# Kernel optimization log

Measured on AMD Instinct MI355X. Metric: run time of the kernel, lower is better.

The kernel has to match this reference:

```python
import jax, jax.numpy as jnp
import numpy as np

N = 100000          # neurons
MAX_DELAY = 5
NSYN = 5            # synaptic basis functions
T = 20              # timesteps
B = 1
E_REC = 2_000_000
N_LGN = 17400
E_LGN = 600_000
N_BKG = 100
E_BKG = 200_000
DT = 1.0
DAMPENING = 0.3
REC_DAMPENING = 0.4


@jax.custom_vjp
def spike(v_scaled, damp):
    return (v_scaled > 0.0).astype(v_scaled.dtype)

def _spike_fwd(v_scaled, damp):
    return spike(v_scaled, damp), (v_scaled, damp)

def _spike_bwd(res, dy):
    v_scaled, damp = res
    dv = dy * damp * jnp.maximum(1.0 - jnp.abs(v_scaled), 0.0)
    return dv, jnp.zeros_like(damp)

spike.defvjp(_spike_fwd, _spike_bwd)


def _sparse_current(spk, idx, w, fac, n_out):
    # spk: [B, S]; idx: [E, 2] (post, pre); w: [E]; fac: [E, NSYN] -> [B, n_out, NSYN]
    vals = spk[:, idx[:, 1]]                                 # [B, E] gather
    contrib = vals[:, :, None] * (w[:, None] * fac)[None]    # [B, E, NSYN]
    seg = lambda c: jax.ops.segment_sum(c, idx[:, 0], num_segments=n_out)
    return jax.vmap(seg)(contrib)


def setup_inputs():
    key = jax.random.key(0)
    ks = jax.random.split(key, 24)
    lgn_spikes = (jax.random.uniform(ks[0], (T, B, N_LGN)) < 0.05).astype(jnp.float32)
    bkg_spikes = (jax.random.uniform(ks[1], (T, B, N_BKG)) < 0.10).astype(jnp.float32)
    post = jax.random.randint(ks[2], (E_REC,), 0, N)
    pre = jax.random.randint(ks[3], (E_REC,), 0, N)
    delay = jax.random.randint(ks[4], (E_REC,), 1, MAX_DELAY + 1)
    rec_indices = jnp.stack([post, pre + N * (delay - 1)], axis=1)  # delayed column offset
    rec_w = jax.random.normal(ks[5], (E_REC,)) * 0.01
    rec_factors = jax.random.uniform(ks[6], (E_REC, NSYN))
    lgn_indices = jnp.stack([jax.random.randint(ks[7], (E_LGN,), 0, N),
                             jax.random.randint(ks[8], (E_LGN,), 0, N_LGN)], axis=1)
    lgn_w = jnp.abs(jax.random.normal(ks[9], (E_LGN,))) * 0.02
    lgn_factors = jax.random.uniform(ks[10], (E_LGN, NSYN))
    bkg_indices = jnp.stack([jax.random.randint(ks[11], (E_BKG,), 0, N),
                             jax.random.randint(ks[12], (E_BKG,), 0, N_BKG)], axis=1)
    bkg_w = jnp.abs(jax.random.normal(ks[13], (E_BKG,))) * 0.02
    bkg_factors = jax.random.uniform(ks[14], (E_BKG, NSYN))
    # GLIF neuron params in normalized voltage units (E_L=0, V_th=1 after scaling)
    tau = jax.random.uniform(ks[15], (N,)) * 30.0 + 10.0      # membrane tau (ms)
    c_m = jax.random.uniform(ks[16], (N,)) * 150.0 + 50.0     # capacitance
    decay = jnp.exp(-DT / tau)
    current_factor = (1.0 - decay) * tau / c_m
    v_reset = jnp.zeros((N,), jnp.float32)
    t_ref = jax.random.uniform(ks[17], (N,)) * 3.0 + 1.0
    k = jax.random.uniform(ks[18], (N, 2)) * 0.3 + 0.003      # ASC decay rates
    asc_amps = jax.random.normal(ks[19], (N, 2)) * 0.01
    v_th = jnp.ones((N,), jnp.float32)
    normalizer = jnp.ones((N,), jnp.float32)                   # v_th - e_l
    gathered_g = jnp.zeros((N,), jnp.float32)                  # g * e_l (= 0 normalized)
    tau_syn = jnp.array([5.5, 8.5, 2.8, 5.8, 1.0], jnp.float32)  # tau_basis.npy
    syn_decay = jnp.exp(-DT / tau_syn)
    psc_initial = jnp.float32(np.e) / tau_syn
    return dict(lgn_spikes=lgn_spikes, bkg_spikes=bkg_spikes,
                rec_indices=rec_indices, rec_w=rec_w, rec_factors=rec_factors,
                lgn_indices=lgn_indices, lgn_w=lgn_w, lgn_factors=lgn_factors,
                bkg_indices=bkg_indices, bkg_w=bkg_w, bkg_factors=bkg_factors,
                decay=decay, current_factor=current_factor, v_reset=v_reset,
                t_ref=t_ref, k=k, asc_amps=asc_amps, v_th=v_th,
                normalizer=normalizer, gathered_g=gathered_g,
                syn_decay=syn_decay, psc_initial=psc_initial)


def reference(lgn_spikes, bkg_spikes, rec_indices, rec_w, rec_factors,
              lgn_indices, lgn_w, lgn_factors, bkg_indices, bkg_w, bkg_factors,
              decay, current_factor, v_reset, t_ref, k, asc_amps, v_th,
              normalizer, gathered_g, syn_decay, psc_initial):
    damp = jnp.float32(DAMPENING)

    def step(carry, xt):
        zbuf, v, r, asc, psc_rise, psc = carry
        lgn_t, bkg_t = xt
        prev_z = zbuf[:, :N]
        # recurrent-dampened spikes for gradient (forward value unchanged)
        dz = REC_DAMPENING * zbuf + (1.0 - REC_DAMPENING) * jax.lax.stop_gradient(zbuf)
        rec_in = _sparse_current(dz, rec_indices, rec_w, rec_factors, N)
        ext_in = (_sparse_current(lgn_t, lgn_indices, lgn_w, lgn_factors, N)
                  + _sparse_current(bkg_t, bkg_indices, bkg_w, bkg_factors, N))
        inp = rec_in + ext_in                                   # [B, N, NSYN]
        new_psc_rise = psc_rise * syn_decay + inp * psc_initial
        new_psc = psc * syn_decay + DT * syn_decay * psc_rise
        input_current = jnp.sum(psc, axis=-1)                   # [B, N]
        c1 = input_current + jnp.sum(asc, axis=-1) + gathered_g
        decayed_v = decay * v + current_factor * c1
        new_v = jnp.where(prev_z > 0.5, v_reset, decayed_v)     # hard reset
        new_r = jnp.clip(r + prev_z * t_ref - DT, 0.0, t_ref)
        new_asc = jnp.exp(-DT * k) * asc + prev_z[..., None] * asc_amps
        v_sc = (new_v - v_th) / normalizer
        z = spike(v_sc, damp)
        new_z = jnp.where(new_r > 0.0, jnp.zeros_like(z), z)    # refractory mask
        new_zbuf = jnp.concatenate([new_z, zbuf[:, :-N]], axis=1)
        return (new_zbuf, new_v, new_r, new_asc, new_psc_rise, new_psc), new_z

    carry0 = (jnp.zeros((B, N * MAX_DELAY), jnp.float32),
              jnp.zeros((B, N), jnp.float32),
              jnp.zeros((B, N), jnp.float32),
              jnp.zeros((B, N, 2), jnp.float32),
              jnp.zeros((B, N, NSYN), jnp.float32),
              jnp.zeros((B, N, NSYN), jnp.float32))
    _, zs = jax.lax.scan(step, carry0, (lgn_spikes, bkg_spikes))
    return zs  # [T, B, N]
```

## Files before the change

### kernel.cpp

```cpp
#include <hip/hip_runtime.h>

#define N_NEURONS 100000
#define MAX_DELAY 5
#define NSYN 5
#define T_STEPS 20
#define N_LGN 17400
#define N_BKG 100
#define N_SRC (N_LGN + N_BKG)
#define E_REC 2000000
#define E_LGN 600000
#define E_BKG 200000
#define E_EXT (E_LGN + E_BKG)
#define DT 1.0f
#define NN_PER_BLK 64
#define NTGT 1563
#define DIRW (NTGT + 1)
#define NCHUNK 512
#define CHUNK 1563
#define RUNW (CHUNK * 4)
#define ASTR 21
#define SCALE_F 262144.0f
#define INV_SCALE (1.0 / 262144.0)

#define OFF_FLAG   0u
#define OFF_BITS   32u
#define OFF_DIR    17536u
#define OFF_RUNS   818304u
#define OFF_ZBUF   4019328u
#define OFF_V      4519328u
#define OFF_R      4619328u
#define OFF_ASC    4719328u
#define OFF_PR     4919328u
#define OFF_PC     5419328u
#define OFF_INPI   5919328u

__global__ void prep(const float* __restrict__ lgn, const float* __restrict__ bkg,
                     unsigned* __restrict__ bits, int* __restrict__ zp) {
    int tid = blockIdx.x * blockDim.x + threadIdx.x;
    if (tid < 32) zp[tid] = 0;
    int i = tid - 32;
    if (i < 0 || i >= N_SRC) return;
    unsigned b = 0;
    if (i < N_LGN) {
#pragma unroll
        for (int t = 0; t < T_STEPS; ++t)
            if (lgn[t * N_LGN + i] != 0.0f) b |= (1u << t);
    } else {
        int j = i - N_LGN;
#pragma unroll
        for (int t = 0; t < T_STEPS; ++t)
            if (bkg[t * N_BKG + j] != 0.0f) b |= (1u << t);
    }
    bits[i] = b;
}

__global__ void __launch_bounds__(1024) sort_pack(
    const int* __restrict__ lgn_idx, const float* __restrict__ lgn_w,
    const float* __restrict__ lgn_fac,
    const int* __restrict__ bkg_idx, const float* __restrict__ bkg_w,
    const float* __restrict__ bkg_fac,
    const unsigned* __restrict__ bits,
    int* __restrict__ dir, int* __restrict__ runs)
{
    __shared__ int hist[NTGT];
    __shared__ int cur[NTGT];
    __shared__ int wsum[16];
    int tid = threadIdx.x, c = blockIdx.x;
    int e0 = c * CHUNK;
    int e1 = e0 + CHUNK; if (e1 > E_EXT) e1 = E_EXT;

    for (int i = tid; i < NTGT; i += 1024) hist[i] = 0;

    int w00 = 0, w10 = 0, w20 = 0, w30 = 0, h0 = 0; bool a0v = false;
    int w01 = 0, w11 = 0, w21 = 0, w31 = 0, h1 = 0; bool a1v = false;
    {
        int e = e0 + tid;
        if (e < e1) {
            int post, srow;
            if (e < E_LGN) { int2 p = ((const int2*)lgn_idx)[e]; post = p.x; srow = p.y; }
            else           { int2 p = ((const int2*)bkg_idx)[e - E_LGN]; post = p.x; srow = N_LGN + p.y; }
            unsigned m = bits[srow];
            if (m) {
                float w; const float* f;
                if (e < E_LGN) { w = lgn_w[e]; f = lgn_fac + 5 * (size_t)e; }
                else { int b = e - E_LGN; w = bkg_w[b]; f = bkg_fac + 5 * (size_t)b; }
                float wsc = w * SCALE_F;
                int q0 = __float2int_rn(wsc * f[0]);
                int q1 = __float2int_rn(wsc * f[1]);
                int q2 = __float2int_rn(wsc * f[2]);
                int q3 = __float2int_rn(wsc * f[3]);
                int q4 = __float2int_rn(wsc * f[4]);
                w00 = (int)(m | ((unsigned)(post & 63) << 20));
                w10 = q0 | (q1 << 16);
                w20 = q2 | (q3 << 16);
                w30 = q4;
                h0 = post >> 6; a0v = true;
            }
        }
    }
    {
        int e = e0 + tid + 1024;
        if (e < e1) {
            int post, srow;
            if (e < E_LGN) { int2 p = ((const int2*)lgn_idx)[e]; post = p.x; srow = p.y; }
            else           { int2 p = ((const int2*)bkg_idx)[e - E_LGN]; post = p.x; srow = N_LGN + p.y; }
            unsigned m = bits[srow];
            if (m) {
                float w; const float* f;
                if (e < E_LGN) { w = lgn_w[e]; f = lgn_fac + 5 * (size_t)e; }
                else { int b = e - E_LGN; w = bkg_w[b]; f = bkg_fac + 5 * (size_t)b; }
                float wsc = w * SCALE_F;
                int q0 = __float2int_rn(wsc * f[0]);
                int q1 = __float2int_rn(wsc * f[1]);
                int q2 = __float2int_rn(wsc * f[2]);
                int q3 = __float2int_rn(wsc * f[3]);
                int q4 = __float2int_rn(wsc * f[4]);
                w01 = (int)(m | ((unsigned)(post & 63) << 20));
                w11 = q0 | (q1 << 16);
                w21 = q2 | (q3 << 16);
                w31 = q4;
                h1 = post >> 6; a1v = true;
            }
        }
    }
    __syncthreads();

    if (a0v) atomicAdd(&hist[h0], 1);
    if (a1v) atomicAdd(&hist[h1], 1);
    __syncthreads();

    int base = tid * 2;
    int v0 = (base < NTGT) ? hist[base] : 0;
    int v1 = (base + 1 < NTGT) ? hist[base + 1] : 0;
    int s = v0 + v1;
    int lane = tid & 63, wid = tid >> 6;
    int inc = s;
#pragma unroll
    for (int off = 1; off < 64; off <<= 1) {
        int v = __shfl_up(inc, off);
        if (lane >= off) inc += v;
    }
    if (lane == 63) wsum[wid] = inc;
    __syncthreads();
    if (tid < 16) {
        int x = wsum[tid];
        int i2 = x;
#pragma unroll
        for (int off = 1; off < 16; off <<= 1) {
            int u = __shfl_up(i2, off);
            if (tid >= off) i2 += u;
        }
        wsum[tid] = i2 - x;
    }
    __syncthreads();
    int excl = wsum[wid] + (inc - s);
    if (base < NTGT) {
        cur[base] = excl;
        dir[(size_t)c * DIRW + base] = excl;
    }
    if (base + 1 <= NTGT) {
        if (base + 1 < NTGT) cur[base + 1] = excl + v0;
        dir[(size_t)c * DIRW + base + 1] = excl + v0;
    }
    __syncthreads();

    int* run = runs + (size_t)c * RUNW;
    if (a0v) {
        int slot = atomicAdd(&cur[h0], 1);
        *(int4*)(run + (size_t)slot * 4) = make_int4(w00, w10, w20, w30);
    }
    if (a1v) {
        int slot = atomicAdd(&cur[h1], 1);
        *(int4*)(run + (size_t)slot * 4) = make_int4(w01, w11, w21, w31);
    }
}

__global__ void __launch_bounds__(256) fused_scan(
    const int* __restrict__ dir, const int* __restrict__ runs,
    const float* __restrict__ decay, const float* __restrict__ cf,
    const float* __restrict__ vres, const float* __restrict__ tref,
    const float* __restrict__ kk, const float* __restrict__ aamps,
    const float* __restrict__ vth, const float* __restrict__ norm,
    const float* __restrict__ gg, const float* __restrict__ sdec,
    const float* __restrict__ psci,
    float* __restrict__ out, int* __restrict__ flag)
{
    __shared__ unsigned long long a01[NN_PER_BLK * ASTR];
    __shared__ unsigned long long a23[NN_PER_BLK * ASTR];
    __shared__ unsigned a4[NN_PER_BLK * ASTR];
    int tid = threadIdx.x;
    int b = blockIdx.x;
    int n0 = b * NN_PER_BLK;

    for (int i = tid; i < NN_PER_BLK * ASTR; i += 256) { a01[i] = 0ull; a23[i] = 0ull; a4[i] = 0u; }
    __syncthreads();

    for (int cc = tid; cc < NCHUNK; cc += 256) {
        const int* dp = dir + (size_t)cc * DIRW + b;
        int d0 = dp[0], d1 = dp[1];
        const int* run = runs + (size_t)cc * RUNW;
        for (int k = d0; k < d1; ++k) {
            int4 r = *(const int4*)(run + (size_t)k * 4);
            unsigned w0 = (unsigned)r.x;
            unsigned m = w0 & 0xFFFFFu;
            int pl = (int)(w0 >> 20);
            unsigned long long q01 = (unsigned long long)((unsigned)r.y & 0xFFFFu)
                                   | ((unsigned long long)((unsigned)r.y >> 16) << 32);
            unsigned long long q23 = (unsigned long long)((unsigned)r.z & 0xFFFFu)
                                   | ((unsigned long long)((unsigned)r.z >> 16) << 32);
            unsigned q4v = (unsigned)r.w;
            int basei = pl * ASTR;
            while (m) {
                int t = __ffs(m) - 1;
                m &= m - 1;
                atomicAdd(&a01[basei + t], q01);
                atomicAdd(&a23[basei + t], q23);
                atomicAdd(&a4[basei + t], q4v);
            }
        }
    }
    __syncthreads();

    if (tid >= NN_PER_BLK) return;
    int n = n0 + tid;
    if (n >= N_NEURONS) return;

    float dec = decay[n], cfa = cf[n], vr = vres[n], tr = tref[n];
    float ek0 = expf(-DT * kk[2 * n]), ek1 = expf(-DT * kk[2 * n + 1]);
    float aa0 = aamps[2 * n], aa1 = aamps[2 * n + 1];
    float vt = vth[n], nm = norm[n], g = gg[n];
    float sd0 = sdec[0], sd1 = sdec[1], sd2 = sdec[2], sd3 = sdec[3], sd4 = sdec[4];
    float pi0 = psci[0], pi1 = psci[1], pi2 = psci[2], pi3 = psci[3], pi4 = psci[4];

    float pr0 = 0.f, pr1 = 0.f, pr2 = 0.f, pr3 = 0.f, pr4 = 0.f;
    float pc0 = 0.f, pc1 = 0.f, pc2 = 0.f, pc3 = 0.f, pc4 = 0.f;
    float v = 0.f, r = 0.f, a0 = 0.f, a1 = 0.f, pz = 0.f;
    bool anyf = false;
    int basei = tid * ASTR;

#pragma unroll
    for (int t = 0; t < T_STEPS; ++t) {
        float ic = pc0 + pc1 + pc2 + pc3 + pc4;
        float c1 = ic + a0 + a1 + g;
        float dv = dec * v + cfa * c1;
        float nv = (pz > 0.5f) ? vr : dv;
        float nr = r + pz * tr - DT;
        nr = fminf(fmaxf(nr, 0.0f), tr);
        a0 = ek0 * a0 + pz * aa0;
        a1 = ek1 * a1 + pz * aa1;

        unsigned long long v01 = a01[basei + t];
        unsigned long long v23 = a23[basei + t];
        float i0 = (float)((double)(unsigned)(v01 & 0xFFFFFFFFull) * INV_SCALE);
        float i1 = (float)((double)(unsigned)(v01 >> 32) * INV_SCALE);
        float i2 = (float)((double)(unsigned)(v23 & 0xFFFFFFFFull) * INV_SCALE);
        float i3 = (float)((double)(unsigned)(v23 >> 32) * INV_SCALE);
        float i4 = (float)((double)a4[basei + t] * INV_SCALE);

        float np0 = pc0 * sd0 + DT * sd0 * pr0;
        float np1 = pc1 * sd1 + DT * sd1 * pr1;
        float np2 = pc2 * sd2 + DT * sd2 * pr2;
        float np3 = pc3 * sd3 + DT * sd3 * pr3;
        float np4 = pc4 * sd4 + DT * sd4 * pr4;
        pr0 = pr0 * sd0 + i0 * pi0;  pc0 = np0;
        pr1 = pr1 * sd1 + i1 * pi1;  pc1 = np1;
        pr2 = pr2 * sd2 + i2 * pi2;  pc2 = np2;
        pr3 = pr3 * sd3 + i3 * pi3;  pc3 = np3;
        pr4 = pr4 * sd4 + i4 * pi4;  pc4 = np4;

        v = nv; r = nr;
        float vsc = (nv - vt) / nm;
        float z = (vsc > 0.0f) ? 1.0f : 0.0f;
        float nz = (nr > 0.0f) ? 0.0f : z;
        out[(size_t)t * N_NEURONS + n] = nz;
        pz = nz;
        anyf = anyf || (nz != 0.0f);
    }
    if (anyf) atomicAdd(flag, 1);
}

__global__ void __launch_bounds__(1024) fallback_redo(
    const int* __restrict__ dir, const int* __restrict__ runs,
    const int* __restrict__ rec_idx, const float* __restrict__ rec_w,
    const float* __restrict__ rec_fac,
    const float* __restrict__ decay, const float* __restrict__ cf,
    const float* __restrict__ vres, const float* __restrict__ tref,
    const float* __restrict__ kk, const float* __restrict__ aamps,
    const float* __restrict__ vth, const float* __restrict__ norm,
    const float* __restrict__ gg, const float* __restrict__ sdec,
    const float* __restrict__ psci,
    float* __restrict__ zbuf, float* __restrict__ vv, float* __restrict__ rr,
    float* __restrict__ asc, float* __restrict__ pra, float* __restrict__ pca,
    int* __restrict__ inpi, float* __restrict__ out, const int* __restrict__ flag)
{
    if (flag[0] == 0) return;
    int tid = threadIdx.x;
    for (int i = tid; i < N_NEURONS; i += 1024) { vv[i] = 0.f; rr[i] = 0.f; }
    for (int i = tid; i < 2 * N_NEURONS; i += 1024) asc[i] = 0.f;
    for (int i = tid; i < NSYN * N_NEURONS; i += 1024) { pra[i] = 0.f; pca[i] = 0.f; }
    for (int i = tid; i < MAX_DELAY * N_NEURONS; i += 1024) zbuf[i] = 0.f;
    __syncthreads();

    for (int t = 0; t < T_STEPS; ++t) {
        for (int i = tid; i < NSYN * N_NEURONS; i += 1024) inpi[i] = 0;
        __syncthreads();
        for (int cc = tid; cc < NCHUNK; cc += 1024) {
            const int* dp  = dir + (size_t)cc * DIRW;
            const int* run = runs + (size_t)cc * RUNW;
            for (int b2 = 0; b2 < NTGT; ++b2) {
                int d0 = dp[b2], d1 = dp[b2 + 1];
                for (int k = d0; k < d1; ++k) {
                    int4 r = *(const int4*)(run + (size_t)k * 4);
                    unsigned w0 = (unsigned)r.x;
                    if ((w0 >> t) & 1u) {
                        int post = b2 * NN_PER_BLK + (int)(w0 >> 20);
                        atomicAdd(&inpi[post * NSYN + 0], (int)((unsigned)r.y & 0xFFFFu));
                        atomicAdd(&inpi[post * NSYN + 1], (int)((unsigned)r.y >> 16));
                        atomicAdd(&inpi[post * NSYN + 2], (int)((unsigned)r.z & 0xFFFFu));
                        atomicAdd(&inpi[post * NSYN + 3], (int)((unsigned)r.z >> 16));
                        atomicAdd(&inpi[post * NSYN + 4], r.w);
                    }
                }
            }
        }
        __syncthreads();
        if (t > 0) {
            for (int e = tid; e < E_REC; e += 1024) {
                int2 pcol = ((const int2*)rec_idx)[e];
                int post = pcol.x, col = pcol.y;
                int d1 = col / N_NEURONS;
                int pre = col - d1 * N_NEURONS;
                int st = t - 1 - d1;
                if (st < 0) continue;
                if (zbuf[(st % MAX_DELAY) * N_NEURONS + pre] != 0.0f) {
                    float w = rec_w[e];
                    atomicAdd(&inpi[post * NSYN + 0], __float2int_rn(w * rec_fac[5 * e + 0] * SCALE_F));
                    atomicAdd(&inpi[post * NSYN + 1], __float2int_rn(w * rec_fac[5 * e + 1] * SCALE_F));
                    atomicAdd(&inpi[post * NSYN + 2], __float2int_rn(w * rec_fac[5 * e + 2] * SCALE_F));
                    atomicAdd(&inpi[post * NSYN + 3], __float2int_rn(w * rec_fac[5 * e + 3] * SCALE_F));
                    atomicAdd(&inpi[post * NSYN + 4], __float2int_rn(w * rec_fac[5 * e + 4] * SCALE_F));
                }
            }
        }
        __syncthreads();
        for (int n = tid; n < N_NEURONS; n += 1024) {
            float pz = (t == 0) ? 0.f : zbuf[((t - 1) % MAX_DELAY) * N_NEURONS + n];
            float prx[NSYN], pcx[NSYN];
            float ic = 0.f;
#pragma unroll
            for (int s = 0; s < NSYN; ++s) {
                prx[s] = pra[n * NSYN + s];
                pcx[s] = pca[n * NSYN + s];
                ic += pcx[s];
            }
            float a0 = asc[2 * n], a1 = asc[2 * n + 1];
            float c1 = ic + a0 + a1 + gg[n];
            float dv = decay[n] * vv[n] + cf[n] * c1;
            float nv = (pz > 0.5f) ? vres[n] : dv;
            float tr = tref[n];
            float nr = rr[n] + pz * tr - DT;
            nr = fminf(fmaxf(nr, 0.0f), tr);
            asc[2 * n]     = expf(-DT * kk[2 * n])     * a0 + pz * aamps[2 * n];
            asc[2 * n + 1] = expf(-DT * kk[2 * n + 1]) * a1 + pz * aamps[2 * n + 1];
#pragma unroll
            for (int s = 0; s < NSYN; ++s) {
                float is = (float)((double)inpi[n * NSYN + s] * INV_SCALE);
                float sd = sdec[s];
                float np = pcx[s] * sd + DT * sd * prx[s];
                pra[n * NSYN + s] = prx[s] * sd + is * psci[s];
                pca[n * NSYN + s] = np;
            }
            vv[n] = nv; rr[n] = nr;
            float vsc = (nv - vth[n]) / norm[n];
            float z = (vsc > 0.0f) ? 1.0f : 0.0f;
            float nz = (nr > 0.0f) ? 0.0f : z;
            zbuf[(t % MAX_DELAY) * N_NEURONS + n] = nz;
            out[(size_t)t * N_NEURONS + n] = nz;
        }
        __syncthreads();
    }
}

extern "C" void kernel_launch(void* const* d_in, const int* in_sizes, int n_in,
                              void* d_out, int out_size, void* d_ws, size_t ws_size,
                              hipStream_t stream) {
    const float* lgn_spikes  = (const float*)d_in[0];
    const float* bkg_spikes  = (const float*)d_in[1];
    const int*   rec_indices = (const int*)  d_in[2];
    const float* rec_w       = (const float*)d_in[3];
    const float* rec_factors = (const float*)d_in[4];
    const int*   lgn_indices = (const int*)  d_in[5];
    const float* lgn_w       = (const float*)d_in[6];
    const float* lgn_factors = (const float*)d_in[7];
    const int*   bkg_indices = (const int*)  d_in[8];
    const float* bkg_w       = (const float*)d_in[9];
    const float* bkg_factors = (const float*)d_in[10];
    const float* decay       = (const float*)d_in[11];
    const float* current_factor = (const float*)d_in[12];
    const float* v_reset     = (const float*)d_in[13];
    const float* t_ref       = (const float*)d_in[14];
    const float* k           = (const float*)d_in[15];
    const float* asc_amps    = (const float*)d_in[16];
    const float* v_th        = (const float*)d_in[17];
    const float* normalizer  = (const float*)d_in[18];
    const float* gathered_g  = (const float*)d_in[19];
    const float* syn_decay   = (const float*)d_in[20];
    const float* psc_initial = (const float*)d_in[21];

    float* ws = (float*)d_ws;
    int*      flag = (int*)(ws + OFF_FLAG);
    unsigned* bits = (unsigned*)(ws + OFF_BITS);
    int*      dir  = (int*)(ws + OFF_DIR);
    int*      runs = (int*)(ws + OFF_RUNS);
    float*    zbuf = ws + OFF_ZBUF;
    float*    vv   = ws + OFF_V;
    float*    rr   = ws + OFF_R;
    float*    asc  = ws + OFF_ASC;
    float*    pra  = ws + OFF_PR;
    float*    pca  = ws + OFF_PC;
    int*      inpi = (int*)(ws + OFF_INPI);
    float*    out  = (float*)d_out;

    prep<<<(32 + N_SRC + 255) / 256, 256, 0, stream>>>(lgn_spikes, bkg_spikes, bits, flag);
    sort_pack<<<NCHUNK, 1024, 0, stream>>>(
        lgn_indices, lgn_w, lgn_factors, bkg_indices, bkg_w, bkg_factors,
        bits, dir, runs);
    fused_scan<<<NTGT, 256, 0, stream>>>(
        dir, runs,
        decay, current_factor, v_reset, t_ref, k, asc_amps,
        v_th, normalizer, gathered_g, syn_decay, psc_initial,
        out, flag);
    fallback_redo<<<1, 1024, 0, stream>>>(
        dir, runs, rec_indices, rec_w, rec_factors,
        decay, current_factor, v_reset, t_ref, k, asc_amps,
        v_th, normalizer, gathered_g, syn_decay, psc_initial,
        zbuf, vv, rr, asc, pra, pca, inpi, out, flag);
}
```

Baseline: 46.68 us.

## Halve chunk count, stage sorted runs in LDS, remap blocks per XCD

Cuts the number of edge chunks from 512 to 256, so each sort block handles 3125 edges. Weight/factor loads are deferred until after the histogram and done only for active edges. Sorted records are staged in shared memory and written out contiguously with coalesced stores. In fused_scan each thread now owns exactly one chunk, halving per-block directory lookups, and block ids are remapped so neighbouring target blocks land on the same XCD for L2 locality. The cost is a larger shared-memory footprint in sort_pack and more work per thread.

```diff
diff --git a/kernel.cpp b/kernel.cpp
--- a/kernel.cpp
+++ b/kernel.cpp
@@ -15,8 +15,8 @@
 #define NN_PER_BLK 64
 #define NTGT 1563
 #define DIRW (NTGT + 1)
-#define NCHUNK 512
-#define CHUNK 1563
+#define NCHUNK 256
+#define CHUNK 3125
 #define RUNW (CHUNK * 4)
 #define ASTR 21
 #define SCALE_F 262144.0f
@@ -25,14 +25,14 @@
 #define OFF_FLAG   0u
 #define OFF_BITS   32u
 #define OFF_DIR    17536u
-#define OFF_RUNS   818304u
-#define OFF_ZBUF   4019328u
-#define OFF_V      4519328u
-#define OFF_R      4619328u
-#define OFF_ASC    4719328u
-#define OFF_PR     4919328u
-#define OFF_PC     5419328u
-#define OFF_INPI   5919328u
+#define OFF_RUNS   417920u
+#define OFF_ZBUF   3617920u
+#define OFF_V      4117920u
+#define OFF_R      4217920u
+#define OFF_ASC    4317920u
+#define OFF_PR     4517920u
+#define OFF_PC     5017920u
+#define OFF_INPI   5517920u
 
 __global__ void prep(const float* __restrict__ lgn, const float* __restrict__ bkg,
                      unsigned* __restrict__ bits, int* __restrict__ zp) {
@@ -65,68 +65,32 @@
     __shared__ int hist[NTGT];
     __shared__ int cur[NTGT];
     __shared__ int wsum[16];
+    __shared__ int totS;
+    __shared__ int4 stage[CHUNK];
     int tid = threadIdx.x, c = blockIdx.x;
     int e0 = c * CHUNK;
-    int e1 = e0 + CHUNK; if (e1 > E_EXT) e1 = E_EXT;
 
     for (int i = tid; i < NTGT; i += 1024) hist[i] = 0;
 
-    int w00 = 0, w10 = 0, w20 = 0, w30 = 0, h0 = 0; bool a0v = false;
-    int w01 = 0, w11 = 0, w21 = 0, w31 = 0, h1 = 0; bool a1v = false;
-    {
-        int e = e0 + tid;
-        if (e < e1) {
+    unsigned mm[4];
+    int pp[4];
+#pragma unroll
+    for (int k = 0; k < 4; ++k) {
+        mm[k] = 0; pp[k] = 0;
+        int e = e0 + tid + k * 1024;
+        if (e < e0 + CHUNK) {
             int post, srow;
             if (e < E_LGN) { int2 p = ((const int2*)lgn_idx)[e]; post = p.x; srow = p.y; }
             else           { int2 p = ((const int2*)bkg_idx)[e - E_LGN]; post = p.x; srow = N_LGN + p.y; }
             unsigned m = bits[srow];
-            if (m) {
-                float w; const float* f;
-                if (e < E_LGN) { w = lgn_w[e]; f = lgn_fac + 5 * (size_t)e; }
-                else { int b = e - E_LGN; w = bkg_w[b]; f = bkg_fac + 5 * (size_t)b; }
-                float wsc = w * SCALE_F;
-                int q0 = __float2int_rn(wsc * f[0]);
-                int q1 = __float2int_rn(wsc * f[1]);
-                int q2 = __float2int_rn(wsc * f[2]);
-                int q3 = __float2int_rn(wsc * f[3]);
-                int q4 = __float2int_rn(wsc * f[4]);
-                w00 = (int)(m | ((unsigned)(post & 63) << 20));
-                w10 = q0 | (q1 << 16);
-                w20 = q2 | (q3 << 16);
-                w30 = q4;
-                h0 = post >> 6; a0v = true;
-            }
-        }
-    }
-    {
-        int e = e0 + tid + 1024;
-        if (e < e1) {
-            int post, srow;
-            if (e < E_LGN) { int2 p = ((const int2*)lgn_idx)[e]; post = p.x; srow = p.y; }
-            else           { int2 p = ((const int2*)bkg_idx)[e - E_LGN]; post = p.x; srow = N_LGN + p.y; }
-            unsigned m = bits[srow];
-            if (m) {
-                float w; const float* f;
-                if (e < E_LGN) { w = lgn_w[e]; f = lgn_fac + 5 * (size_t)e; }
-                else { int b = e - E_LGN; w = bkg_w[b]; f = bkg_fac + 5 * (size_t)b; }
-                float wsc = w * SCALE_F;
-                int q0 = __float2int_rn(wsc * f[0]);
-                int q1 = __float2int_rn(wsc * f[1]);
-                int q2 = __float2int_rn(wsc * f[2]);
-                int q3 = __float2int_rn(wsc * f[3]);
-                int q4 = __float2int_rn(wsc * f[4]);
-                w01 = (int)(m | ((unsigned)(post & 63) << 20));
-                w11 = q0 | (q1 << 16);
-                w21 = q2 | (q3 << 16);
-                w31 = q4;
-                h1 = post >> 6; a1v = true;
-            }
-        }
-    }
-    __syncthreads();
-
-    if (a0v) atomicAdd(&hist[h0], 1);
-    if (a1v) atomicAdd(&hist[h1], 1);
+            if (m) { mm[k] = m; pp[k] = post; }
+        }
+    }
+    __syncthreads();
+
+#pragma unroll
+    for (int k = 0; k < 4; ++k)
+        if (mm[k]) atomicAdd(&hist[pp[k] >> 6], 1);
     __syncthreads();
 
     int base = tid * 2;
@@ -160,19 +124,35 @@
     }
     if (base + 1 <= NTGT) {
         if (base + 1 < NTGT) cur[base + 1] = excl + v0;
+        else totS = excl + v0;
         dir[(size_t)c * DIRW + base + 1] = excl + v0;
     }
     __syncthreads();
 
+#pragma unroll
+    for (int k = 0; k < 4; ++k) {
+        if (mm[k]) {
+            int e = e0 + tid + k * 1024;
+            float w; const float* f;
+            if (e < E_LGN) { w = lgn_w[e]; f = lgn_fac + 5 * (size_t)e; }
+            else { int b = e - E_LGN; w = bkg_w[b]; f = bkg_fac + 5 * (size_t)b; }
+            float wsc = w * SCALE_F;
+            int q0 = __float2int_rn(wsc * f[0]);
+            int q1 = __float2int_rn(wsc * f[1]);
+            int q2 = __float2int_rn(wsc * f[2]);
+            int q3 = __float2int_rn(wsc * f[3]);
+            int q4 = __float2int_rn(wsc * f[4]);
+            int slot = atomicAdd(&cur[pp[k] >> 6], 1);
+            stage[slot] = make_int4((int)(mm[k] | ((unsigned)(pp[k] & 63) << 20)),
+                                    q0 | (q1 << 16), q2 | (q3 << 16), q4);
+        }
+    }
+    __syncthreads();
+
+    int tot = totS;
     int* run = runs + (size_t)c * RUNW;
-    if (a0v) {
-        int slot = atomicAdd(&cur[h0], 1);
-        *(int4*)(run + (size_t)slot * 4) = make_int4(w00, w10, w20, w30);
-    }
-    if (a1v) {
-        int slot = atomicAdd(&cur[h1], 1);
-        *(int4*)(run + (size_t)slot * 4) = make_int4(w01, w11, w21, w31);
-    }
+    for (int k2 = tid; k2 < tot; k2 += 1024)
+        *(int4*)(run + (size_t)k2 * 4) = stage[k2];
 }
 
 __global__ void __launch_bounds__(256) fused_scan(
@@ -189,13 +169,16 @@
     __shared__ unsigned long long a23[NN_PER_BLK * ASTR];
     __shared__ unsigned a4[NN_PER_BLK * ASTR];
     int tid = threadIdx.x;
-    int b = blockIdx.x;
+    int bid = blockIdx.x;
+    int xcd = bid & 7, idx = bid >> 3;
+    int b = (xcd < 3) ? (xcd * 196 + idx) : (588 + (xcd - 3) * 195 + idx);
     int n0 = b * NN_PER_BLK;
 
     for (int i = tid; i < NN_PER_BLK * ASTR; i += 256) { a01[i] = 0ull; a23[i] = 0ull; a4[i] = 0u; }
     __syncthreads();
 
-    for (int cc = tid; cc < NCHUNK; cc += 256) {
+    {
+        int cc = tid;
         const int* dp = dir + (size_t)cc * DIRW + b;
         int d0 = dp[0], d1 = dp[1];
         const int* run = runs + (size_t)cc * RUNW;
@@ -304,9 +287,9 @@
     for (int t = 0; t < T_STEPS; ++t) {
         for (int i = tid; i < NSYN * N_NEURONS; i += 1024) inpi[i] = 0;
         __syncthreads();
-        for (int cc = tid; cc < NCHUNK; cc += 1024) {
-            const int* dp  = dir + (size_t)cc * DIRW;
-            const int* run = runs + (size_t)cc * RUNW;
+        if (tid < NCHUNK) {
+            const int* dp  = dir + (size_t)tid * DIRW;
+            const int* run = runs + (size_t)tid * RUNW;
             for (int b2 = 0; b2 < NTGT; ++b2) {
                 int d0 = dp[b2], d1 = dp[b2 + 1];
                 for (int k = d0; k < d1; ++k) {
```

After: 40.12 us. -14.1%, faster.
